# Performance work log

Hardware: AMD Instinct MI355X
Metric: run time of the kernel (lower is better)

## Reference

```python
import jax, jax.numpy as jnp
import numpy as np

M, NC, NT, DX = 8, 1024, 512, 3
CHUNK = 512          # chunk_size
N_STEPS = 8          # n_steps (tol=0.0 -> torch early-stop never fires)
LR = 0.1
B1, B2, EPS = 0.9, 0.999, 1e-8
SQRT5 = 5.0 ** 0.5
LOG2PI = float(np.log(2.0 * np.pi))
NOISE_LB = 1e-4      # gpytorch GreaterThan(1e-4) noise constraint


def setup_inputs():
    key = jax.random.key(0)
    k1, k2, k3 = jax.random.split(key, 3)
    return {
        "xc": jax.random.normal(k1, (M, NC, DX), jnp.float32),
        "yc": jax.random.normal(k2, (M, NC, 1), jnp.float32),
        "xt": jax.random.normal(k3, (M, NT, DX), jnp.float32),
    }


def _kernel(x1, x2, ls, outscale):
    # ScaleKernel(MaternKernel(nu=2.5)); ls: [m,1,1], outscale: [m]
    xs1, xs2 = x1 / ls, x2 / ls
    d2 = (jnp.sum(xs1 * xs1, -1)[:, :, None]
          + jnp.sum(xs2 * xs2, -1)[:, None, :]
          - 2.0 * jnp.einsum('mnd,mkd->mnk', xs1, xs2))
    d2 = jnp.clip(d2, 1e-12, None)   # clamp like gpytorch dist for grad safety
    d = jnp.sqrt(d2)
    k = (1.0 + SQRT5 * d + (5.0 / 3.0) * d2) * jnp.exp(-SQRT5 * d)
    return outscale[:, None, None] * k


def _constrained(params):
    ls = jax.nn.softplus(params["raw_ls"])                          # [m,1,1]
    outscale = jax.nn.softplus(params["raw_os"])                    # [m]
    noise = jax.nn.softplus(params["raw_noise"][:, 0]) + NOISE_LB   # [m]
    return ls, outscale, noise


def _nll(params, x, y):
    # sum over tasks of -ExactMarginalLogLikelihood (gpytorch divides by n)
    ls, outscale, noise = _constrained(params)
    n = x.shape[1]
    K = _kernel(x, x, ls, outscale) + noise[:, None, None] * jnp.eye(n, dtype=x.dtype)
    L = jnp.linalg.cholesky(K)
    diff = y - params["const"][:, None]
    alpha = jax.scipy.linalg.cho_solve((L, True), diff[..., None])[..., 0]
    quad = jnp.sum(diff * alpha, -1)
    logdet = 2.0 * jnp.sum(jnp.log(jnp.diagonal(L, axis1=-2, axis2=-1)), -1)
    mll = -0.5 * (quad + logdet + n * LOG2PI) / n
    return jnp.sum(-mll)


def _adam_step(carry, x_sub, y_sub):
    p, m_, v_, t = carry
    g = jax.grad(_nll)(p, x_sub, y_sub)
    t = t + 1.0
    tm = jax.tree_util.tree_map
    m_ = tm(lambda a, gg: B1 * a + (1.0 - B1) * gg, m_, g)
    v_ = tm(lambda a, gg: B2 * a + (1.0 - B2) * gg * gg, v_, g)
    bc1 = 1.0 - B1 ** t
    bc2 = 1.0 - B2 ** t
    p = tm(lambda pp, mm, vv: pp - LR * (mm / bc1) / (jnp.sqrt(vv / bc2) + EPS), p, m_, v_)
    return (p, m_, v_, t)


def _gp_forward(xc, yc, xt):
    y = yc[..., 0]                                    # [m, nc]
    zl = lambda s: jnp.zeros(s, jnp.float32)
    # gpytorch raw params initialize to 0
    params = {"raw_ls": zl((M, 1, 1)), "raw_os": zl((M,)),
              "raw_noise": zl((M, 1)), "const": zl((M,))}
    m_ = jax.tree_util.tree_map(jnp.zeros_like, params)
    v_ = jax.tree_util.tree_map(jnp.zeros_like, params)
    carry = (params, m_, v_, jnp.float32(0.0))
    for i in range(0, NC, CHUNK):                     # 'Expanding' strategy
        end = min(i + CHUNK, NC)
        x_sub, y_sub = xc[:, :end], y[:, :end]
        step = lambda c, _: (_adam_step(c, x_sub, y_sub), None)
        carry, _ = jax.lax.scan(step, carry, None, length=N_STEPS)
    params = carry[0]
    # posterior predictive with trained hypers (train data = full context)
    ls, outscale, noise = _constrained(params)
    Kcc = _kernel(xc, xc, ls, outscale) + noise[:, None, None] * jnp.eye(NC, dtype=xc.dtype)
    L = jnp.linalg.cholesky(Kcc)
    diff = y - params["const"][:, None]
    alpha = jax.scipy.linalg.cho_solve((L, True), diff[..., None])[..., 0]
    Ktc = _kernel(xt, xc, ls, outscale)               # [m, nt, nc]
    mean = params["const"][:, None] + jnp.einsum('mtn,mn->mt', Ktc, alpha)
    v = jax.scipy.linalg.solve_triangular(L, jnp.swapaxes(Ktc, 1, 2), lower=True)  # [m,nc,nt]
    var_f = outscale[:, None] - jnp.sum(v * v, axis=1)  # Matern(0)=1 -> prior diag = outputscale
    var = var_f + noise[:, None]                      # likelihood(f) adds observation noise
    return jnp.stack([mean, var])                     # [2, m, nt]


def reference(xc, yc, xt):
    return _gp_forward(xc, yc, xt)
```

## Files before the change

kernel.cpp:

```cpp
#include <hip/hip_runtime.h>
#include <math.h>

constexpr int MM = 8;
constexpr int NC = 1024;
constexpr int NT = 512;

constexpr size_t OFF_A     = (size_t)MM * 1024 * 1024;
constexpr size_t OFF_T     = OFF_A * 2;
constexpr size_t OFF_KTC   = OFF_T + (size_t)MM * 512 * 512;
constexpr size_t OFF_ALPHA = OFF_KTC + (size_t)MM * NT * NC;
constexpr size_t OFF_SCAL  = OFF_ALPHA + (size_t)MM * 1024;
constexpr size_t OFF_ACC   = OFF_SCAL + (size_t)MM * 32;
constexpr size_t OFF_CTR   = OFF_ACC + (size_t)MM * 8;

#define S5 2.2360679775f

__device__ __forceinline__ float sigmf(float x) { return 1.0f / (1.0f + expf(-x)); }
__device__ __forceinline__ float softplusf(float x) { return fmaxf(x, 0.0f) + log1pf(expf(-fabsf(x))); }

__device__ __forceinline__ void lt_decode(int x, int& i, int& j) {
  int ii = 0;
  while ((ii + 1) * (ii + 2) / 2 <= x) ++ii;
  i = ii; j = x - ii * (ii + 1) / 2;
}

struct SMem {
  float Ls[64 * 65];
  float Us[64 * 65];
  float Tt[32 * 33];
  float dvec[64];
  float As[16][68];
  float Bs[16][68];
  float xi[64][3];
  float xj[64][3];
  float ai[64];
  float aj[64];
  float red[4][4];
};

template <int TA, int TB>
__device__ __forceinline__ void gemm64(const float* __restrict__ A, int lda,
                                       const float* __restrict__ B, int ldb,
                                       int kBeg, int kEnd, float acc[4][4], SMem& sm) {
  int tid = threadIdx.x, tx = tid & 15, ty = tid >> 4;
  float ra[4], rb[4];
  auto ldAB = [&](int k0) {
#pragma unroll
    for (int q = 0; q < 4; ++q) {
      int e = tid + (q << 8);
      if (TA) { int kk = e >> 6, r = e & 63; ra[q] = A[(size_t)(k0 + kk) * lda + r]; }
      else    { int r = e >> 4, kk = e & 15; ra[q] = A[(size_t)r * lda + k0 + kk]; }
      if (TB) { int c = e >> 4, kk = e & 15; rb[q] = B[(size_t)c * ldb + k0 + kk]; }
      else    { int kk = e >> 6, c = e & 63; rb[q] = B[(size_t)(k0 + kk) * ldb + c]; }
    }
  };
  ldAB(kBeg);
  for (int k0 = kBeg; k0 < kEnd; k0 += 16) {
    __syncthreads();
#pragma unroll
    for (int q = 0; q < 4; ++q) {
      int e = tid + (q << 8);
      if (TA) sm.As[e >> 6][e & 63] = ra[q]; else sm.As[e & 15][e >> 4] = ra[q];
      if (TB) sm.Bs[e & 15][e >> 4] = rb[q]; else sm.Bs[e >> 6][e & 63] = rb[q];
    }
    __syncthreads();
    if (k0 + 16 < kEnd) ldAB(k0 + 16);
#pragma unroll
    for (int kk = 0; kk < 16; ++kk) {
      float a[4], b[4];
#pragma unroll
      for (int i = 0; i < 4; ++i) a[i] = sm.As[kk][ty * 4 + i];
#pragma unroll
      for (int j = 0; j < 4; ++j) b[j] = sm.Bs[kk][tx * 4 + j];
#pragma unroll
      for (int i = 0; i < 4; ++i)
#pragma unroll
        for (int j = 0; j < 4; ++j) acc[i][j] = fmaf(a[i], b[j], acc[i][j]);
    }
  }
}

__device__ void factor64(SMem& sm, float* Uout, int ldu) {
  int tid = threadIdx.x;
  int tx = tid & 15, ty = tid >> 4;
  for (int j = 0; j < 63; ++j) {
    float rinv = 1.0f / sm.Ls[j * 65 + j];
    for (int i = j + 1 + ty; i < 64; i += 16) {
      float lij = sm.Ls[i * 65 + j] * rinv;
      for (int c = j + 1 + tx; c <= i; c += 16) sm.Ls[i * 65 + c] -= lij * sm.Ls[c * 65 + j];
    }
    __syncthreads();
  }
  if (tid < 64) sm.dvec[tid] = 1.0f / sqrtf(sm.Ls[tid * 65 + tid]);
  __syncthreads();
  for (int e = tid; e < 4096; e += 256) { int r = e >> 6, c = e & 63; if (c <= r) sm.Ls[r * 65 + c] *= sm.dvec[c]; }
  __syncthreads();
  for (int e = tid; e < 64 * 65; e += 256) sm.Us[e] = 0.0f;
  __syncthreads();
  if (tid < 64) {
    int b = tid >> 5, c0 = tid & 31, base = b * 32, gc = base + c0;
    sm.Us[gc * 65 + gc] = 1.0f / sm.Ls[gc * 65 + gc];
    for (int r = c0 + 1; r < 32; ++r) {
      int gr = base + r;
      float acc = 0.0f;
      for (int l = c0; l < r; ++l) acc += sm.Ls[gr * 65 + base + l] * sm.Us[(base + l) * 65 + gc];
      sm.Us[gr * 65 + gc] = -acc / sm.Ls[gr * 65 + gr];
    }
  }
  __syncthreads();
  for (int e = tid; e < 1024; e += 256) {
    int r = e >> 5, c = e & 31;
    float acc = 0.0f;
    for (int l = c; l < 32; ++l) acc += sm.Ls[(32 + r) * 65 + l] * sm.Us[l * 65 + c];
    sm.Tt[r * 33 + c] = acc;
  }
  __syncthreads();
  for (int e = tid; e < 1024; e += 256) {
    int r = e >> 5, c = e & 31;
    float acc = 0.0f;
    for (int l = 0; l <= r; ++l) acc += sm.Us[(32 + r) * 65 + 32 + l] * sm.Tt[l * 33 + c];
    sm.Us[(32 + r) * 65 + c] = -acc;
  }
  __syncthreads();
  for (int e = tid; e < 4096; e += 256) { int r = e >> 6, c = e & 63; Uout[(size_t)r * ldu + c] = sm.Us[r * 65 + c]; }
}


__global__ __launch_bounds__(256) void k_init(float* ws) {
  int t = threadIdx.x;
  float* scal = ws + OFF_SCAL;
  float* acc = ws + OFF_ACC;
  if (t < MM) {
    float* s = scal + t * 32;
    for (int i = 0; i < 12; ++i) s[i] = 0.0f;
    float sp0 = 0.69314718056f;
    s[12] = sp0; s[13] = sp0; s[14] = sp0 + 1e-4f; s[15] = 0.0f;
  }
  if (t < MM * 8) acc[t] = 0.0f;
  if (t < MM) ((unsigned*)(ws + OFF_CTR))[t] = 0u;
}

__global__ __launch_bounds__(256) void k_buildK(const float* __restrict__ xc, float* ws, int n) {
  __shared__ SMem sm;
  int job = blockIdx.x, m = blockIdx.y, tid = threadIdx.x;
  const float* xm = xc + (size_t)m * NC * 3;
  float* Km = ws + (size_t)m * 1048576;
  float* Am = ws + OFF_A + (size_t)m * 1048576;
  const float* sT = ws + OFF_SCAL + m * 32;
  float ls = sT[12], os = sT[13], noi = sT[14];
  float il2 = 1.0f / (ls * ls);
  if (job >= 1 && job <= 4) {
    int zi = (job - 1) * 256 + tid;
    if (zi < n) ws[OFF_ALPHA + (size_t)m * 1024 + zi] = 0.0f;
  }
  if (job == 5) {
    if (tid < 4) ws[OFF_ACC + m * 8 + tid] = 0.0f;
    if (tid == 4) ((unsigned*)(ws + OFF_CTR))[m] = 0u;
  }
  int bi, bj; lt_decode(job, bi, bj);
  if (tid < 64) {
    int r = bi * 64 + tid;
    sm.xi[tid][0] = xm[r * 3 + 0]; sm.xi[tid][1] = xm[r * 3 + 1]; sm.xi[tid][2] = xm[r * 3 + 2];
  } else if (tid < 128) {
    int lr = tid - 64; int r = bj * 64 + lr;
    sm.xj[lr][0] = xm[r * 3 + 0]; sm.xj[lr][1] = xm[r * 3 + 1]; sm.xj[lr][2] = xm[r * 3 + 2];
  }
  __syncthreads();
  if (job == 0) {
    for (int e = tid; e < 4096; e += 256) {
      int r = e >> 6, c = e & 63;
      float d0 = sm.xi[r][0] - sm.xj[c][0], d1 = sm.xi[r][1] - sm.xj[c][1], d2 = sm.xi[r][2] - sm.xj[c][2];
      float r2 = d0 * d0 + d1 * d1 + d2 * d2;
      float z = fmaxf(r2 * il2, 1e-12f);
      float dd = sqrtf(z);
      float kv = os * (1.0f + S5 * dd + (5.0f / 3.0f) * z) * __expf(-S5 * dd);
      if (r == c) kv += noi;
      sm.Ls[r * 65 + c] = kv;
    }
    __syncthreads();
    factor64(sm, Am, n);
  } else {
    for (int e = tid; e < 4096; e += 256) {
      int r = e >> 6, c = e & 63;
      float d0 = sm.xi[r][0] - sm.xj[c][0], d1 = sm.xi[r][1] - sm.xj[c][1], d2 = sm.xi[r][2] - sm.xj[c][2];
      float r2 = d0 * d0 + d1 * d1 + d2 * d2;
      float z = fmaxf(r2 * il2, 1e-12f);
      float dd = sqrtf(z);
      float kv = os * (1.0f + S5 * dd + (5.0f / 3.0f) * z) * __expf(-S5 * dd);
      if (bi == bj && r == c) kv += noi;
      Km[(size_t)(bi * 64 + r) * n + bj * 64 + c] = kv;
    }
  }
}

__global__ __launch_bounds__(256) void k_trail(float* ws, int k, int n) {
  __shared__ SMem sm;
  int job = blockIdx.x, m = blockIdx.y, tid = threadIdx.x;
  int tx = tid & 15, ty = tid >> 4;
  float* Km = ws + (size_t)m * 1048576;
  float* Am = ws + OFF_A + (size_t)m * 1048576;
  const float* Linv = Am + (size_t)(k * 64) * n + k * 64;
  int di, dj; lt_decode(job, di, dj);
  int i = k + 1 + di, j = k + 1 + dj;
  float pp[4][4] = {};
  gemm64<0, 1>(Km + (size_t)(i * 64) * n + k * 64, n, Linv, n, 0, 64, pp, sm);
  __syncthreads();
#pragma unroll
  for (int ii = 0; ii < 4; ++ii)
#pragma unroll
    for (int jj = 0; jj < 4; ++jj) sm.Ls[(ty * 4 + ii) * 65 + tx * 4 + jj] = pp[ii][jj];
  if (di == dj) {
    float* P = Am + (size_t)(i * 64) * n + k * 64;
#pragma unroll
    for (int ii = 0; ii < 4; ++ii)
#pragma unroll
      for (int jj = 0; jj < 4; ++jj) P[(size_t)(ty * 4 + ii) * n + tx * 4 + jj] = pp[ii][jj];
  } else {
#pragma unroll
    for (int ii = 0; ii < 4; ++ii)
#pragma unroll
      for (int jj = 0; jj < 4; ++jj) pp[ii][jj] = 0.0f;
    gemm64<0, 1>(Km + (size_t)(j * 64) * n + k * 64, n, Linv, n, 0, 64, pp, sm);
#pragma unroll
    for (int ii = 0; ii < 4; ++ii)
#pragma unroll
      for (int jj = 0; jj < 4; ++jj) sm.Us[(ty * 4 + ii) * 65 + tx * 4 + jj] = pp[ii][jj];
  }
  __syncthreads();
  float acc[4][4] = {};
  {
    const float* Bsrc = (di == dj) ? sm.Ls : sm.Us;
    for (int l = 0; l < 64; ++l) {
      float a[4], b[4];
#pragma unroll
      for (int ii = 0; ii < 4; ++ii) a[ii] = sm.Ls[(ty * 4 + ii) * 65 + l];
#pragma unroll
      for (int jj = 0; jj < 4; ++jj) b[jj] = Bsrc[(tx * 4 + jj) * 65 + l];
#pragma unroll
      for (int ii = 0; ii < 4; ++ii)
#pragma unroll
        for (int jj = 0; jj < 4; ++jj) acc[ii][jj] = fmaf(a[ii], b[jj], acc[ii][jj]);
    }
  }
  float* C = Km + (size_t)(i * 64) * n + j * 64;
  if (job == 0) {
    __syncthreads();
#pragma unroll
    for (int ii = 0; ii < 4; ++ii)
#pragma unroll
      for (int jj = 0; jj < 4; ++jj)
        sm.Ls[(ty * 4 + ii) * 65 + tx * 4 + jj] =
            C[(size_t)(ty * 4 + ii) * n + tx * 4 + jj] - acc[ii][jj];
    __syncthreads();
    factor64(sm, Am + (size_t)((k + 1) * 64) * n + (k + 1) * 64, n);
  } else {
#pragma unroll
    for (int ii = 0; ii < 4; ++ii)
#pragma unroll
      for (int jj = 0; jj < 4; ++jj)
        C[(size_t)(ty * 4 + ii) * n + tx * 4 + jj] -= acc[ii][jj];
  }
}

__global__ __launch_bounds__(256) void k_trinv64(float* ws, int n) {
  __shared__ SMem sm;
  int p = blockIdx.x, m = blockIdx.y, tid = threadIdx.x;
  int tx = tid & 15, ty = tid >> 4;
  float* Am = ws + OFF_A + (size_t)m * 1048576;
  int rb = (2 * p + 1) * 64, cb = 2 * p * 64;
  for (int e = tid; e < 4096; e += 256) {
    int r = e >> 6, c = e & 63;
    sm.Ls[r * 65 + c] = Am[(size_t)(rb + r) * n + cb + c];
    sm.Us[r * 65 + c] = Am[(size_t)(cb + r) * n + cb + c];
  }
  __syncthreads();
  float tt[4][4] = {};
  for (int l = 0; l < 64; ++l) {
    float a[4], b[4];
#pragma unroll
    for (int ii = 0; ii < 4; ++ii) a[ii] = sm.Ls[(ty * 4 + ii) * 65 + l];
#pragma unroll
    for (int jj = 0; jj < 4; ++jj) b[jj] = sm.Us[l * 65 + tx * 4 + jj];
#pragma unroll
    for (int ii = 0; ii < 4; ++ii)
#pragma unroll
      for (int jj = 0; jj < 4; ++jj) tt[ii][jj] = fmaf(a[ii], b[jj], tt[ii][jj]);
  }
  __syncthreads();
#pragma unroll
  for (int ii = 0; ii < 4; ++ii)
#pragma unroll
    for (int jj = 0; jj < 4; ++jj) sm.Ls[(ty * 4 + ii) * 65 + tx * 4 + jj] = tt[ii][jj];
  for (int e = tid; e < 4096; e += 256) {
    int r = e >> 6, c = e & 63;
    sm.Us[r * 65 + c] = Am[(size_t)(rb + r) * n + rb + c];
  }
  __syncthreads();
  float oo[4][4] = {};
  for (int l = 0; l < 64; ++l) {
    float a[4], b[4];
#pragma unroll
    for (int ii = 0; ii < 4; ++ii) a[ii] = sm.Us[(ty * 4 + ii) * 65 + l];
#pragma unroll
    for (int jj = 0; jj < 4; ++jj) b[jj] = sm.Ls[l * 65 + tx * 4 + jj];
#pragma unroll
    for (int ii = 0; ii < 4; ++ii)
#pragma unroll
      for (int jj = 0; jj < 4; ++jj) oo[ii][jj] = fmaf(a[ii], b[jj], oo[ii][jj]);
  }
#pragma unroll
  for (int ii = 0; ii < 4; ++ii)
#pragma unroll
    for (int jj = 0; jj < 4; ++jj)
      Am[(size_t)(rb + ty * 4 + ii) * n + cb + tx * 4 + jj] = -oo[ii][jj];
}

__global__ __launch_bounds__(256) void k_trinvT(float* ws, int s, int n) {
  __shared__ SMem sm;
  int job = blockIdx.x, m = blockIdx.y;
  int tx = threadIdx.x & 15, ty = threadIdx.x >> 4;
  float* Am = ws + OFF_A + (size_t)m * 1048576;
  float* Tm = ws + OFF_T + (size_t)m * 262144;
  int st = s >> 6;
  int p = job / (st * st), rem = job % (st * st);
  int ti = rem / st, tj = rem % st;
  int base = p * 2 * s;
  float acc[4][4] = {};
  gemm64<0, 0>(Am + (size_t)(base + s + ti * 64) * n + base, n,
               Am + (size_t)base * n + base + tj * 64, n, tj * 64, s, acc, sm);
  float* C = Tm + (size_t)p * s * s + (size_t)(ti * 64) * s + tj * 64;
#pragma unroll
  for (int ii = 0; ii < 4; ++ii)
#pragma unroll
    for (int jj = 0; jj < 4; ++jj) C[(size_t)(ty * 4 + ii) * s + tx * 4 + jj] = acc[ii][jj];
}

__global__ __launch_bounds__(256) void k_trinvA(float* ws, int s, int n) {
  __shared__ SMem sm;
  int job = blockIdx.x, m = blockIdx.y;
  int tx = threadIdx.x & 15, ty = threadIdx.x >> 4;
  float* Am = ws + OFF_A + (size_t)m * 1048576;
  const float* Tm = ws + OFF_T + (size_t)m * 262144;
  int st = s >> 6;
  int p = job / (st * st), rem = job % (st * st);
  int ti = rem / st, tj = rem % st;
  int base = p * 2 * s;
  float acc[4][4] = {};
  gemm64<0, 0>(Am + (size_t)(base + s + ti * 64) * n + base + s, n,
               Tm + (size_t)p * s * s + tj * 64, s, 0, (ti + 1) * 64, acc, sm);
  float* C = Am + (size_t)(base + s + ti * 64) * n + base + tj * 64;
#pragma unroll
  for (int ii = 0; ii < 4; ++ii)
#pragma unroll
    for (int jj = 0; jj < 4; ++jj) C[(size_t)(ty * 4 + ii) * n + tx * 4 + jj] = -acc[ii][jj];
}

__global__ __launch_bounds__(256) void k_syrkAT(const float* __restrict__ yc, float* ws, int n) {
  __shared__ SMem sm;
  int job = blockIdx.x, m = blockIdx.y, tid = threadIdx.x;
  int tx = tid & 15, ty = tid >> 4;
  const float* Am = ws + OFF_A + (size_t)m * 1048576;
  float* Gm = ws + (size_t)m * 1048576;
  const float* ym = yc + (size_t)m * NC;
  float* accp = ws + OFF_ACC + m * 8;
  float* al = ws + OFF_ALPHA + (size_t)m * 1024;
  float cm = ws[OFF_SCAL + m * 32 + 15];
  int ib, jb; lt_decode(job, ib, jb);
  if (tid < 64) sm.ai[tid] = ym[ib * 64 + tid] - cm;
  else if (tid < 128) sm.aj[tid - 64] = ym[jb * 64 + tid - 64] - cm;
  float acc[4][4] = {};
  gemm64<1, 0>(Am + ib * 64, n, Am + jb * 64, n, ib * 64, n, acc, sm);
#pragma unroll
  for (int ii = 0; ii < 4; ++ii)
#pragma unroll
    for (int jj = 0; jj < 4; ++jj) {
      int r = ty * 4 + ii, c = tx * 4 + jj;
      Gm[(size_t)(ib * 64 + r) * n + jb * 64 + c] = acc[ii][jj];
      if (ib != jb) Gm[(size_t)(jb * 64 + c) * n + ib * 64 + r] = acc[ii][jj];
    }
  if (ib == jb && tx == ty) {
    atomicAdd(&accp[2], acc[0][0] + acc[1][1] + acc[2][2] + acc[3][3]);
  }
  float rowp[4];
#pragma unroll
  for (int i = 0; i < 4; ++i) {
    float s = 0.0f;
#pragma unroll
    for (int j = 0; j < 4; ++j) s = fmaf(acc[i][j], sm.aj[tx * 4 + j], s);
    rowp[i] = s;
  }
  float colp[4];
  if (ib != jb) {
#pragma unroll
    for (int j = 0; j < 4; ++j) {
      float s = 0.0f;
#pragma unroll
      for (int i = 0; i < 4; ++i) s = fmaf(acc[i][j], sm.ai[ty * 4 + i], s);
      colp[j] = s;
    }
  }
  __syncthreads();
  float* redA = &sm.As[0][0];
  float* redB = &sm.Bs[0][0];
#pragma unroll
  for (int i = 0; i < 4; ++i) redA[(ty * 4 + i) * 16 + tx] = rowp[i];
  if (ib != jb) {
#pragma unroll
    for (int j = 0; j < 4; ++j) redB[(tx * 4 + j) * 16 + ty] = colp[j];
  }
  __syncthreads();
  if (tid < 64) {
    float s = 0.0f;
#pragma unroll
    for (int q = 0; q < 16; ++q) s += redA[tid * 16 + q];
    atomicAdd(&al[ib * 64 + tid], s);
    if (ib != jb) {
      float s2 = 0.0f;
#pragma unroll
      for (int q = 0; q < 16; ++q) s2 += redB[tid * 16 + q];
      atomicAdd(&al[jb * 64 + tid], s2);
    }
  }
}

__global__ __launch_bounds__(256) void k_reduceAD(const float* __restrict__ xc,
                                                  const float* __restrict__ yc,
                                                  float* ws, int n, int tstep) {
  __shared__ SMem sm;
  __shared__ unsigned tkt;
  int job = blockIdx.x, m = blockIdx.y, tid = threadIdx.x;
  const float* xm = xc + (size_t)m * NC * 3;
  const float* Gm = ws + (size_t)m * 1048576;
  const float* al = ws + OFF_ALPHA + (size_t)m * 1024;
  float* accp = ws + OFF_ACC + m * 8;
  float* sT = ws + OFF_SCAL + m * 32;
  int nb = n >> 6;
  int njobs = nb * (nb + 1) / 2;
  float ls = sT[12], os = sT[13];
  float il2 = 1.0f / (ls * ls);
  float c53 = (5.0f / 3.0f) * os / ls;
  int bi, bj; lt_decode(job, bi, bj);
  float w = (bi == bj) ? 1.0f : 2.0f;
  if (tid < 64) {
    int r = bi * 64 + tid;
    sm.xi[tid][0] = xm[r * 3 + 0]; sm.xi[tid][1] = xm[r * 3 + 1]; sm.xi[tid][2] = xm[r * 3 + 2];
    sm.ai[tid] = al[r];
  } else if (tid < 128) {
    int lr = tid - 64; int r = bj * 64 + lr;
    sm.xj[lr][0] = xm[r * 3 + 0]; sm.xj[lr][1] = xm[r * 3 + 1]; sm.xj[lr][2] = xm[r * 3 + 2];
    sm.aj[lr] = al[r];
  }
  __syncthreads();
  float a1 = 0.0f, a2 = 0.0f;
// ... 44 lines not shown
    t6 = sm.red[0][2] + sm.red[1][2] + sm.red[2][2] + sm.red[3][2];
    float T1 = __hip_atomic_fetch_add(&accp[0], 0.0f, __ATOMIC_RELAXED, __HIP_MEMORY_SCOPE_AGENT);
    float T2 = __hip_atomic_fetch_add(&accp[1], 0.0f, __ATOMIC_RELAXED, __HIP_MEMORY_SCOPE_AGENT);
    float t3 = __hip_atomic_fetch_add(&accp[2], 0.0f, __ATOMIC_RELAXED, __HIP_MEMORY_SCOPE_AGENT);
    float noi = sT[14];
    float fn = (float)n;
    float g_ls = 0.5f / fn * (T1 - T2);
    float g_os = 0.5f / (fn * os) * (fn - noi * t3 - t6 + noi * t4);
    float g_no = 0.5f / fn * (t3 - t4);
    float g_c = -t5 / fn;
    float gr[4];
    gr[0] = g_ls * sigmf(sT[0]);
    gr[1] = g_os * sigmf(sT[1]);
    gr[2] = g_no * sigmf(sT[2]);
    gr[3] = g_c;
    float bc1 = 1.0f - powf(0.9f, (float)tstep);
    float bc2 = 1.0f - powf(0.999f, (float)tstep);
#pragma unroll
    for (int i = 0; i < 4; ++i) {
      float mv = 0.9f * sT[4 + i] + 0.1f * gr[i];
      float vv = 0.999f * sT[8 + i] + 0.001f * gr[i] * gr[i];
      sT[4 + i] = mv; sT[8 + i] = vv;
      sT[i] = sT[i] - 0.1f * (mv / bc1) / (sqrtf(vv / bc2) + 1e-8f);
    }
    sT[12] = softplusf(sT[0]);
    sT[13] = softplusf(sT[1]);
    sT[14] = softplusf(sT[2]) + 1e-4f;
    sT[15] = sT[3];
  }
}

__global__ __launch_bounds__(256) void k_buildKtc(const float* __restrict__ xt,
                                                  const float* __restrict__ xc, float* ws) {
  __shared__ SMem sm;
  int job = blockIdx.x, m = blockIdx.y, tid = threadIdx.x;
  const float* xtm = xt + (size_t)m * NT * 3;
  const float* xm = xc + (size_t)m * NC * 3;
  float* Kt = ws + OFF_KTC + (size_t)m * NT * NC;
  float* Tm = ws + OFF_T + (size_t)m * 262144;
  const float* sT = ws + OFF_SCAL + m * 32;
  float ls = sT[12], os = sT[13];
  float il2 = 1.0f / (ls * ls);
  if (job < 2) {
    int z = job * 256 + tid;
    Tm[z] = 0.0f; Tm[NT + z] = 0.0f;
  }
  int ti = job >> 4, tj = job & 15;
  if (tid < 64) {
    int r = ti * 64 + tid;
    sm.xi[tid][0] = xtm[r * 3 + 0]; sm.xi[tid][1] = xtm[r * 3 + 1]; sm.xi[tid][2] = xtm[r * 3 + 2];
  } else if (tid < 128) {
    int lr = tid - 64; int r = tj * 64 + lr;
    sm.xj[lr][0] = xm[r * 3 + 0]; sm.xj[lr][1] = xm[r * 3 + 1]; sm.xj[lr][2] = xm[r * 3 + 2];
  }
  __syncthreads();
  for (int e = tid; e < 4096; e += 256) {
    int r = e >> 6, c = e & 63;
    float d0 = sm.xi[r][0] - sm.xj[c][0], d1 = sm.xi[r][1] - sm.xj[c][1], d2 = sm.xi[r][2] - sm.xj[c][2];
    float r2 = d0 * d0 + d1 * d1 + d2 * d2;
    float z = fmaxf(r2 * il2, 1e-12f);
    float dd = sqrtf(z);
    float kv = os * (1.0f + S5 * dd + (5.0f / 3.0f) * z) * __expf(-S5 * dd);
    Kt[(size_t)(ti * 64 + r) * NC + tj * 64 + c] = kv;
  }
}

__global__ __launch_bounds__(256) void k_predW(float* ws) {
  __shared__ SMem sm;
  int job = blockIdx.x, m = blockIdx.y, tid = threadIdx.x;
  int tx = tid & 15, ty = tid >> 4;
  const float* Kt = ws + OFF_KTC + (size_t)m * NT * NC;
  const float* Gm = ws + (size_t)m * 1048576;
  const float* al = ws + OFF_ALPHA + (size_t)m * 1024;
  float* S1 = ws + OFF_T + (size_t)m * 262144;
  float* S2 = S1 + NT;
  int ti = job >> 4, tj = job & 15;
  if (tid < 64) sm.aj[tid] = al[tj * 64 + tid];
  float acc[4][4] = {};
  gemm64<0, 0>(Kt + (size_t)(ti * 64) * NC, NC, Gm + tj * 64, 1024, 0, 1024, acc, sm);
  float s1p[4], s2p[4];
#pragma unroll
  for (int i = 0; i < 4; ++i) {
    float a1 = 0.0f, a2 = 0.0f;
    const float* kr = Kt + (size_t)(ti * 64 + ty * 4 + i) * NC + tj * 64;
#pragma unroll
    for (int j = 0; j < 4; ++j) {
      float kv = kr[tx * 4 + j];
      a1 = fmaf(kv, sm.aj[tx * 4 + j], a1);
      a2 = fmaf(kv, acc[i][j], a2);
    }
    s1p[i] = a1; s2p[i] = a2;
// ... 10 lines not shown
  if (tid < 64) {
    float a1 = 0.0f, a2 = 0.0f;
#pragma unroll
    for (int q = 0; q < 16; ++q) { a1 += redA[tid * 16 + q]; a2 += redB[tid * 16 + q]; }
    atomicAdd(&S1[ti * 64 + tid], a1);
    atomicAdd(&S2[ti * 64 + tid], a2);
  }
}

__global__ __launch_bounds__(256) void k_final(float* ws, float* out) {
  int m = blockIdx.y, t = blockIdx.x * 256 + threadIdx.x;
  const float* S1 = ws + OFF_T + (size_t)m * 262144;
  const float* S2 = S1 + NT;
  const float* sT = ws + OFF_SCAL + m * 32;
  if (t < NT) {
    out[(size_t)m * NT + t] = sT[15] + S1[t];
    out[(size_t)MM * NT + (size_t)m * NT + t] = sT[13] + sT[14] - S2[t];
  }
}

extern "C" void kernel_launch(void* const* d_in, const int* in_sizes, int n_in,
                              void* d_out, int out_size, void* d_ws, size_t ws_size,
                              hipStream_t stream) {
  const float* xc = (const float*)d_in[0];
  const float* yc = (const float*)d_in[1];
  const float* xt = (const float*)d_in[2];
  float* out = (float*)d_out;
  float* ws = (float*)d_ws;

  k_init<<<dim3(1), dim3(256), 0, stream>>>(ws);

  for (int step = 0; step < 17; ++step) {
    int n = step < 8 ? 512 : 1024;
    int nb = n >> 6;
    k_buildK<<<dim3(nb * (nb + 1) / 2, MM), dim3(256), 0, stream>>>(xc, ws, n);
    for (int k = 0; k <= nb - 2; ++k) {
      int t = nb - 1 - k;
      k_trail<<<dim3(t * (t + 1) / 2, MM), dim3(256), 0, stream>>>(ws, k, n);
    }
    k_trinv64<<<dim3(n / 128, MM), dim3(256), 0, stream>>>(ws, n);
    for (int s = 128; s < n; s <<= 1) {
      int st = s >> 6, np = n / (2 * s);
      k_trinvT<<<dim3(np * st * st, MM), dim3(256), 0, stream>>>(ws, s, n);
      k_trinvA<<<dim3(np * st * st, MM), dim3(256), 0, stream>>>(ws, s, n);
    }
    k_syrkAT<<<dim3(nb * (nb + 1) / 2, MM), dim3(256), 0, stream>>>(yc, ws, n);
    if (step < 16) {
      k_reduceAD<<<dim3(nb * (nb + 1) / 2, MM), dim3(256), 0, stream>>>(xc, yc, ws, n, step + 1);
    }
  }

  k_buildKtc<<<dim3(128, MM), dim3(256), 0, stream>>>(xt, xc, ws);
  k_predW<<<dim3(128, MM), dim3(256), 0, stream>>>(ws);
  k_final<<<dim3(2, MM), dim3(256), 0, stream>>>(ws, out);

  (void)in_sizes; (void)n_in; (void)out_size; (void)ws_size;
}
```

Measured before the change: 20.51 ms.

## Switch Cholesky, triangular inverse and SYRK to 128-wide blocks

```diff
diff --git a/kernel.cpp b/kernel.cpp
--- a/kernel.cpp
+++ b/kernel.cpp
@@ -38,6 +38,22 @@
   float red[4][4];
 };
 
+struct SMem128 {
+  float As[16][132];
+  float Bs[16][132];
+  float ai[128];
+  float aj[128];
+  float red[4][4];
+};
+
+struct FactBuf {
+  float Ls[64 * 65];
+  float Us[64 * 65];
+  float P[64 * 65];
+  float Tt[32 * 33];
+  float dvec[64];
+};
+
 template <int TA, int TB>
 __device__ __forceinline__ void gemm64(const float* __restrict__ A, int lda,
                                        const float* __restrict__ B, int ldb,
@@ -80,49 +96,185 @@
   }
 }
 
-__device__ void factor64(SMem& sm, float* Uout, int ldu) {
+template <int TA, int TB>
+__device__ __forceinline__ void gemm128(const float* __restrict__ A, int lda,
+                                        const float* __restrict__ B, int ldb,
+                                        int kBeg, int kEnd, float acc[8][8], SMem128& sm) {
+  int tid = threadIdx.x, tx = tid & 15, ty = tid >> 4;
+  float ra[8], rb[8];
+  auto ldAB = [&](int k0) {
+#pragma unroll
+    for (int q = 0; q < 8; ++q) {
+      int e = tid + (q << 8);
+      if (TA) { int kk = e >> 7, r = e & 127; ra[q] = A[(size_t)(k0 + kk) * lda + r]; }
+      else    { int r = e >> 4, kk = e & 15;  ra[q] = A[(size_t)r * lda + k0 + kk]; }
+      if (TB) { int c = e >> 4, kk = e & 15;  rb[q] = B[(size_t)c * ldb + k0 + kk]; }
+      else    { int kk = e >> 7, c = e & 127; rb[q] = B[(size_t)(k0 + kk) * ldb + c]; }
+    }
+  };
+  ldAB(kBeg);
+  for (int k0 = kBeg; k0 < kEnd; k0 += 16) {
+    __syncthreads();
+#pragma unroll
+    for (int q = 0; q < 8; ++q) {
+      int e = tid + (q << 8);
+      if (TA) sm.As[e >> 7][e & 127] = ra[q]; else sm.As[e & 15][e >> 4] = ra[q];
+      if (TB) sm.Bs[e & 15][e >> 4] = rb[q];  else sm.Bs[e >> 7][e & 127] = rb[q];
+    }
+    __syncthreads();
+    if (k0 + 16 < kEnd) ldAB(k0 + 16);
+#pragma unroll
+    for (int kk = 0; kk < 16; ++kk) {
+      float a[8], b[8];
+#pragma unroll
+      for (int i = 0; i < 8; ++i) a[i] = sm.As[kk][ty * 8 + i];
+#pragma unroll
+      for (int j = 0; j < 8; ++j) b[j] = sm.Bs[kk][tx * 8 + j];
+#pragma unroll
+      for (int i = 0; i < 8; ++i)
+#pragma unroll
+        for (int j = 0; j < 8; ++j) acc[i][j] = fmaf(a[i], b[j], acc[i][j]);
+    }
+  }
+}
+
+__device__ void f64_inlds(float* Ls, float* Us, float* Tt, float* dvec,
+                          float* Uout, int ldu) {
   int tid = threadIdx.x;
   int tx = tid & 15, ty = tid >> 4;
   for (int j = 0; j < 63; ++j) {
-    float rinv = 1.0f / sm.Ls[j * 65 + j];
+    float rinv = 1.0f / Ls[j * 65 + j];
     for (int i = j + 1 + ty; i < 64; i += 16) {
-      float lij = sm.Ls[i * 65 + j] * rinv;
-      for (int c = j + 1 + tx; c <= i; c += 16) sm.Ls[i * 65 + c] -= lij * sm.Ls[c * 65 + j];
+      float lij = Ls[i * 65 + j] * rinv;
+      for (int c = j + 1 + tx; c <= i; c += 16) Ls[i * 65 + c] -= lij * Ls[c * 65 + j];
     }
     __syncthreads();
   }
-  if (tid < 64) sm.dvec[tid] = 1.0f / sqrtf(sm.Ls[tid * 65 + tid]);
-  __syncthreads();
-  for (int e = tid; e < 4096; e += 256) { int r = e >> 6, c = e & 63; if (c <= r) sm.Ls[r * 65 + c] *= sm.dvec[c]; }
-  __syncthreads();
-  for (int e = tid; e < 64 * 65; e += 256) sm.Us[e] = 0.0f;
+  if (tid < 64) dvec[tid] = 1.0f / sqrtf(Ls[tid * 65 + tid]);
+  __syncthreads();
+  for (int e = tid; e < 4096; e += 256) { int r = e >> 6, c = e & 63; if (c <= r) Ls[r * 65 + c] *= dvec[c]; }
+  __syncthreads();
+  for (int e = tid; e < 64 * 65; e += 256) Us[e] = 0.0f;
   __syncthreads();
   if (tid < 64) {
     int b = tid >> 5, c0 = tid & 31, base = b * 32, gc = base + c0;
-    sm.Us[gc * 65 + gc] = 1.0f / sm.Ls[gc * 65 + gc];
+    Us[gc * 65 + gc] = 1.0f / Ls[gc * 65 + gc];
     for (int r = c0 + 1; r < 32; ++r) {
       int gr = base + r;
       float acc = 0.0f;
-      for (int l = c0; l < r; ++l) acc += sm.Ls[gr * 65 + base + l] * sm.Us[(base + l) * 65 + gc];
-      sm.Us[gr * 65 + gc] = -acc / sm.Ls[gr * 65 + gr];
+      for (int l = c0; l < r; ++l) acc += Ls[gr * 65 + base + l] * Us[(base + l) * 65 + gc];
+      Us[gr * 65 + gc] = -acc / Ls[gr * 65 + gr];
     }
   }
   __syncthreads();
   for (int e = tid; e < 1024; e += 256) {
     int r = e >> 5, c = e & 31;
     float acc = 0.0f;
-    for (int l = c; l < 32; ++l) acc += sm.Ls[(32 + r) * 65 + l] * sm.Us[l * 65 + c];
-    sm.Tt[r * 33 + c] = acc;
+    for (int l = c; l < 32; ++l) acc += Ls[(32 + r) * 65 + l] * Us[l * 65 + c];
+    Tt[r * 33 + c] = acc;
   }
   __syncthreads();
   for (int e = tid; e < 1024; e += 256) {
     int r = e >> 5, c = e & 31;
     float acc = 0.0f;
-    for (int l = 0; l <= r; ++l) acc += sm.Us[(32 + r) * 65 + 32 + l] * sm.Tt[l * 33 + c];
-    sm.Us[(32 + r) * 65 + c] = -acc;
-  }
-  __syncthreads();
-  for (int e = tid; e < 4096; e += 256) { int r = e >> 6, c = e & 63; Uout[(size_t)r * ldu + c] = sm.Us[r * 65 + c]; }
+    for (int l = 0; l <= r; ++l) acc += Us[(32 + r) * 65 + 32 + l] * Tt[l * 33 + c];
+    Us[(32 + r) * 65 + c] = -acc;
+  }
+  __syncthreads();
+  for (int e = tid; e < 4096; e += 256) { int r = e >> 6, c = e & 63; Uout[(size_t)r * ldu + c] = Us[r * 65 + c]; }
+}
+
+__device__ void factor128dev(FactBuf& fb, float* Km, float* Am, int r0, int n) {
+  int tid = threadIdx.x, tx = tid & 15, ty = tid >> 4;
+  for (int e = tid; e < 4096; e += 256) { int r = e >> 6, c = e & 63; fb.Ls[r * 65 + c] = Km[(size_t)(r0 + r) * n + r0 + c]; }
+  __syncthreads();
+  f64_inlds(fb.Ls, fb.Us, fb.Tt, fb.dvec, Am + (size_t)r0 * n + r0, n);
+  for (int e = tid; e < 4096; e += 256) { int r = e >> 6, c = e & 63; fb.P[r * 65 + c] = Km[(size_t)(r0 + 64 + r) * n + r0 + c]; }
+  __syncthreads();
+  {
+    float res[4][4] = {};
+    for (int l = 0; l < 64; ++l) {
+      float a[4], b[4];
+#pragma unroll
+      for (int ii = 0; ii < 4; ++ii) a[ii] = fb.P[(ty * 4 + ii) * 65 + l];
+#pragma unroll
+      for (int jj = 0; jj < 4; ++jj) b[jj] = fb.Us[(tx * 4 + jj) * 65 + l];
+#pragma unroll
+      for (int ii = 0; ii < 4; ++ii)
+#pragma unroll
+        for (int jj = 0; jj < 4; ++jj) res[ii][jj] = fmaf(a[ii], b[jj], res[ii][jj]);
+    }
+    __syncthreads();
+#pragma unroll
+    for (int ii = 0; ii < 4; ++ii)
+#pragma unroll
+      for (int jj = 0; jj < 4; ++jj) fb.P[(ty * 4 + ii) * 65 + tx * 4 + jj] = res[ii][jj];
+  }
+  __syncthreads();
+  for (int e = tid; e < 4096; e += 256) { int r = e >> 6, c = e & 63; fb.Ls[r * 65 + c] = Km[(size_t)(r0 + 64 + r) * n + r0 + 64 + c]; }
+  __syncthreads();
+  {
+    float acc[4][4] = {};
+    for (int l = 0; l < 64; ++l) {
+      float a[4], b[4];
+#pragma unroll
+      for (int ii = 0; ii < 4; ++ii) a[ii] = fb.P[(ty * 4 + ii) * 65 + l];
+#pragma unroll
+      for (int jj = 0; jj < 4; ++jj) b[jj] = fb.P[(tx * 4 + jj) * 65 + l];
+#pragma unroll
+      for (int ii = 0; ii < 4; ++ii)
+#pragma unroll
+        for (int jj = 0; jj < 4; ++jj) acc[ii][jj] = fmaf(a[ii], b[jj], acc[ii][jj]);
+    }
+#pragma unroll
+    for (int ii = 0; ii < 4; ++ii)
+#pragma unroll
+      for (int jj = 0; jj < 4; ++jj) fb.Ls[(ty * 4 + ii) * 65 + tx * 4 + jj] -= acc[ii][jj];
+  }
+  __syncthreads();
+  f64_inlds(fb.Ls, fb.Us, fb.Tt, fb.dvec, Am + (size_t)(r0 + 64) * n + r0 + 64, n);
+  for (int e = tid; e < 4096; e += 256) { int r = e >> 6, c = e & 63; fb.Ls[r * 65 + c] = Am[(size_t)(r0 + r) * n + r0 + c]; }
+  __syncthreads();
+  {
+    float res[4][4] = {};
+    for (int l = 0; l < 64; ++l) {
+      float a[4], b[4];
+#pragma unroll
+      for (int ii = 0; ii < 4; ++ii) a[ii] = fb.P[(ty * 4 + ii) * 65 + l];
+#pragma unroll
+      for (int jj = 0; jj < 4; ++jj) b[jj] = fb.Ls[l * 65 + tx * 4 + jj];
+#pragma unroll
+      for (int ii = 0; ii < 4; ++ii)
+#pragma unroll
+        for (int jj = 0; jj < 4; ++jj) res[ii][jj] = fmaf(a[ii], b[jj], res[ii][jj]);
+    }
+    __syncthreads();
+#pragma unroll
+    for (int ii = 0; ii < 4; ++ii)
+#pragma unroll
+      for (int jj = 0; jj < 4; ++jj) fb.P[(ty * 4 + ii) * 65 + tx * 4 + jj] = res[ii][jj];
+  }
+  __syncthreads();
+  {
+    float res[4][4] = {};
+    for (int l = 0; l < 64; ++l) {
+      float a[4], b[4];
+#pragma unroll
+      for (int ii = 0; ii < 4; ++ii) a[ii] = fb.Us[(ty * 4 + ii) * 65 + l];
+#pragma unroll
+      for (int jj = 0; jj < 4; ++jj) b[jj] = fb.P[l * 65 + tx * 4 + jj];
+#pragma unroll
+      for (int ii = 0; ii < 4; ++ii)
+#pragma unroll
+        for (int jj = 0; jj < 4; ++jj) res[ii][jj] = fmaf(a[ii], b[jj], res[ii][jj]);
+    }
+#pragma unroll
+    for (int ii = 0; ii < 4; ++ii)
+#pragma unroll
+      for (int jj = 0; jj < 4; ++jj)
+        Am[(size_t)(r0 + 64 + ty * 4 + ii) * n + r0 + tx * 4 + jj] = -res[ii][jj];
+  }
+  for (int e = tid; e < 4096; e += 256) { int r = e >> 6, c = e & 63; Am[(size_t)(r0 + r) * n + r0 + 64 + c] = 0.0f; }
 }
 
 
@@ -141,11 +293,10 @@
 }
 
 __global__ __launch_bounds__(256) void k_buildK(const float* __restrict__ xc, float* ws, int n) {
-  __shared__ SMem sm;
+  __shared__ float xi[64][3], xj[64][3];
   int job = blockIdx.x, m = blockIdx.y, tid = threadIdx.x;
   const float* xm = xc + (size_t)m * NC * 3;
   float* Km = ws + (size_t)m * 1048576;
-  float* Am = ws + OFF_A + (size_t)m * 1048576;
   const float* sT = ws + OFF_SCAL + m * 32;
   float ls = sT[12], os = sT[13], noi = sT[14];
   float il2 = 1.0f / (ls * ls);
@@ -160,203 +311,111 @@
   int bi, bj; lt_decode(job, bi, bj);
   if (tid < 64) {
     int r = bi * 64 + tid;
-    sm.xi[tid][0] = xm[r * 3 + 0]; sm.xi[tid][1] = xm[r * 3 + 1]; sm.xi[tid][2] = xm[r * 3 + 2];
+    xi[tid][0] = xm[r * 3 + 0]; xi[tid][1] = xm[r * 3 + 1]; xi[tid][2] = xm[r * 3 + 2];
   } else if (tid < 128) {
     int lr = tid - 64; int r = bj * 64 + lr;
-    sm.xj[lr][0] = xm[r * 3 + 0]; sm.xj[lr][1] = xm[r * 3 + 1]; sm.xj[lr][2] = xm[r * 3 + 2];
-  }
-  __syncthreads();
-  if (job == 0) {
-    for (int e = tid; e < 4096; e += 256) {
-      int r = e >> 6, c = e & 63;
-      float d0 = sm.xi[r][0] - sm.xj[c][0], d1 = sm.xi[r][1] - sm.xj[c][1], d2 = sm.xi[r][2] - sm.xj[c][2];
-      float r2 = d0 * d0 + d1 * d1 + d2 * d2;
-      float z = fmaxf(r2 * il2, 1e-12f);
-      float dd = sqrtf(z);
-      float kv = os * (1.0f + S5 * dd + (5.0f / 3.0f) * z) * __expf(-S5 * dd);
-      if (r == c) kv += noi;
-      sm.Ls[r * 65 + c] = kv;
-    }
-    __syncthreads();
-    factor64(sm, Am, n);
-  } else {
-    for (int e = tid; e < 4096; e += 256) {
-      int r = e >> 6, c = e & 63;
-      float d0 = sm.xi[r][0] - sm.xj[c][0], d1 = sm.xi[r][1] - sm.xj[c][1], d2 = sm.xi[r][2] - sm.xj[c][2];
-      float r2 = d0 * d0 + d1 * d1 + d2 * d2;
-      float z = fmaxf(r2 * il2, 1e-12f);
-      float dd = sqrtf(z);
-      float kv = os * (1.0f + S5 * dd + (5.0f / 3.0f) * z) * __expf(-S5 * dd);
-      if (bi == bj && r == c) kv += noi;
-      Km[(size_t)(bi * 64 + r) * n + bj * 64 + c] = kv;
-    }
-  }
-}
-
-__global__ __launch_bounds__(256) void k_trail(float* ws, int k, int n) {
-  __shared__ SMem sm;
-  int job = blockIdx.x, m = blockIdx.y, tid = threadIdx.x;
-  int tx = tid & 15, ty = tid >> 4;
+    xj[lr][0] = xm[r * 3 + 0]; xj[lr][1] = xm[r * 3 + 1]; xj[lr][2] = xm[r * 3 + 2];
+  }
+  __syncthreads();
+  for (int e = tid; e < 4096; e += 256) {
+    int r = e >> 6, c = e & 63;
+    float d0 = xi[r][0] - xj[c][0], d1 = xi[r][1] - xj[c][1], d2 = xi[r][2] - xj[c][2];
+    float r2 = d0 * d0 + d1 * d1 + d2 * d2;
+    float z = fmaxf(r2 * il2, 1e-12f);
+    float dd = sqrtf(z);
+    float kv = os * (1.0f + S5 * dd + (5.0f / 3.0f) * z) * __expf(-S5 * dd);
+    if (bi == bj && r == c) kv += noi;
+    Km[(size_t)(bi * 64 + r) * n + bj * 64 + c] = kv;
+  }
+}
+
+__global__ __launch_bounds__(256) void k_factor128(float* ws, int kk, int n) {
+  __shared__ FactBuf fb;
+  int m = blockIdx.x;
+  factor128dev(fb, ws + (size_t)m * 1048576, ws + OFF_A + (size_t)m * 1048576, kk * 128, n);
+}
+
+__global__ __launch_bounds__(256) void k_panel128(float* ws, int k, int n) {
+  __shared__ SMem128 sm;
+  int m = blockIdx.y, i = k + 1 + blockIdx.x;
+  int tx = threadIdx.x & 15, ty = threadIdx.x >> 4;
   float* Km = ws + (size_t)m * 1048576;
   float* Am = ws + OFF_A + (size_t)m * 1048576;
-  const float* Linv = Am + (size_t)(k * 64) * n + k * 64;
+  float acc[8][8] = {};
+  gemm128<0, 1>(Km + (size_t)(i * 128) * n + k * 128, n,
+                Am + (size_t)(k * 128) * n + k * 128, n, 0, 128, acc, sm);
+  float* P = Am + (size_t)(i * 128) * n + k * 128;
+#pragma unroll
+  for (int ii = 0; ii < 8; ++ii)
+#pragma unroll
+    for (int jj = 0; jj < 8; ++jj) P[(size_t)(ty * 8 + ii) * n + tx * 8 + jj] = acc[ii][jj];
+}
+
+__global__ __launch_bounds__(256) void k_trailF128(float* ws, int k, int n) {
+  __shared__ union { SMem128 g; FactBuf f; } sm;
+  int job = blockIdx.x, m = blockIdx.y;
+  int tx = threadIdx.x & 15, ty = threadIdx.x >> 4;
+  float* Km = ws + (size_t)m * 1048576;
+  float* Am = ws + OFF_A + (size_t)m * 1048576;
   int di, dj; lt_decode(job, di, dj);
   int i = k + 1 + di, j = k + 1 + dj;
-  float pp[4][4] = {};
-  gemm64<0, 1>(Km + (size_t)(i * 64) * n + k * 64, n, Linv, n, 0, 64, pp, sm);
-  __syncthreads();
-#pragma unroll
-  for (int ii = 0; ii < 4; ++ii)
-#pragma unroll
-    for (int jj = 0; jj < 4; ++jj) sm.Ls[(ty * 4 + ii) * 65 + tx * 4 + jj] = pp[ii][jj];
-  if (di == dj) {
-    float* P = Am + (size_t)(i * 64) * n + k * 64;
-#pragma unroll
-    for (int ii = 0; ii < 4; ++ii)
-#pragma unroll
-      for (int jj = 0; jj < 4; ++jj) P[(size_t)(ty * 4 + ii) * n + tx * 4 + jj] = pp[ii][jj];
-  } else {
-#pragma unroll
-    for (int ii = 0; ii < 4; ++ii)
-#pragma unroll
-      for (int jj = 0; jj < 4; ++jj) pp[ii][jj] = 0.0f;
-    gemm64<0, 1>(Km + (size_t)(j * 64) * n + k * 64, n, Linv, n, 0, 64, pp, sm);
-#pragma unroll
-    for (int ii = 0; ii < 4; ++ii)
-#pragma unroll
-      for (int jj = 0; jj < 4; ++jj) sm.Us[(ty * 4 + ii) * 65 + tx * 4 + jj] = pp[ii][jj];
-  }
-  __syncthreads();
-  float acc[4][4] = {};
-  {
-    const float* Bsrc = (di == dj) ? sm.Ls : sm.Us;
-    for (int l = 0; l < 64; ++l) {
-      float a[4], b[4];
-#pragma unroll
-      for (int ii = 0; ii < 4; ++ii) a[ii] = sm.Ls[(ty * 4 + ii) * 65 + l];
-#pragma unroll
-      for (int jj = 0; jj < 4; ++jj) b[jj] = Bsrc[(tx * 4 + jj) * 65 + l];
-#pragma unroll
-      for (int ii = 0; ii < 4; ++ii)
-#pragma unroll
-        for (int jj = 0; jj < 4; ++jj) acc[ii][jj] = fmaf(a[ii], b[jj], acc[ii][jj]);
-    }
-  }
-  float* C = Km + (size_t)(i * 64) * n + j * 64;
+  float acc[8][8] = {};
+  gemm128<0, 1>(Am + (size_t)(i * 128) * n + k * 128, n,
+                Am + (size_t)(j * 128) * n + k * 128, n, 0, 128, acc, sm.g);
+  float* C = Km + (size_t)(i * 128) * n + j * 128;
+#pragma unroll
+  for (int ii = 0; ii < 8; ++ii)
+#pragma unroll
+    for (int jj = 0; jj < 8; ++jj)
+      C[(size_t)(ty * 8 + ii) * n + tx * 8 + jj] -= acc[ii][jj];
   if (job == 0) {
     __syncthreads();
-#pragma unroll
-    for (int ii = 0; ii < 4; ++ii)
-#pragma unroll
-      for (int jj = 0; jj < 4; ++jj)
-        sm.Ls[(ty * 4 + ii) * 65 + tx * 4 + jj] =
-            C[(size_t)(ty * 4 + ii) * n + tx * 4 + jj] - acc[ii][jj];
-    __syncthreads();
-    factor64(sm, Am + (size_t)((k + 1) * 64) * n + (k + 1) * 64, n);
-  } else {
-#pragma unroll
-    for (int ii = 0; ii < 4; ++ii)
-#pragma unroll
-      for (int jj = 0; jj < 4; ++jj)
-        C[(size_t)(ty * 4 + ii) * n + tx * 4 + jj] -= acc[ii][jj];
-  }
-}
-
-__global__ __launch_bounds__(256) void k_trinv64(float* ws, int n) {
-  __shared__ SMem sm;
-  int p = blockIdx.x, m = blockIdx.y, tid = threadIdx.x;
-  int tx = tid & 15, ty = tid >> 4;
-  float* Am = ws + OFF_A + (size_t)m * 1048576;
-  int rb = (2 * p + 1) * 64, cb = 2 * p * 64;
-  for (int e = tid; e < 4096; e += 256) {
-    int r = e >> 6, c = e & 63;
-    sm.Ls[r * 65 + c] = Am[(size_t)(rb + r) * n + cb + c];
-    sm.Us[r * 65 + c] = Am[(size_t)(cb + r) * n + cb + c];
-  }
-  __syncthreads();
-  float tt[4][4] = {};
-  for (int l = 0; l < 64; ++l) {
-    float a[4], b[4];
-#pragma unroll
-    for (int ii = 0; ii < 4; ++ii) a[ii] = sm.Ls[(ty * 4 + ii) * 65 + l];
-#pragma unroll
-    for (int jj = 0; jj < 4; ++jj) b[jj] = sm.Us[l * 65 + tx * 4 + jj];
-#pragma unroll
-    for (int ii = 0; ii < 4; ++ii)
-#pragma unroll
-      for (int jj = 0; jj < 4; ++jj) tt[ii][jj] = fmaf(a[ii], b[jj], tt[ii][jj]);
-  }
-  __syncthreads();
-#pragma unroll
-  for (int ii = 0; ii < 4; ++ii)
-#pragma unroll
-    for (int jj = 0; jj < 4; ++jj) sm.Ls[(ty * 4 + ii) * 65 + tx * 4 + jj] = tt[ii][jj];
-  for (int e = tid; e < 4096; e += 256) {
-    int r = e >> 6, c = e & 63;
-    sm.Us[r * 65 + c] = Am[(size_t)(rb + r) * n + rb + c];
-  }
-  __syncthreads();
-  float oo[4][4] = {};
-  for (int l = 0; l < 64; ++l) {
-    float a[4], b[4];
-#pragma unroll
-    for (int ii = 0; ii < 4; ++ii) a[ii] = sm.Us[(ty * 4 + ii) * 65 + l];
-#pragma unroll
-    for (int jj = 0; jj < 4; ++jj) b[jj] = sm.Ls[l * 65 + tx * 4 + jj];
-#pragma unroll
-    for (int ii = 0; ii < 4; ++ii)
-#pragma unroll
-      for (int jj = 0; jj < 4; ++jj) oo[ii][jj] = fmaf(a[ii], b[jj], oo[ii][jj]);
-  }
-#pragma unroll
-  for (int ii = 0; ii < 4; ++ii)
-#pragma unroll
-    for (int jj = 0; jj < 4; ++jj)
-      Am[(size_t)(rb + ty * 4 + ii) * n + cb + tx * 4 + jj] = -oo[ii][jj];
+    factor128dev(sm.f, Km, Am, (k + 1) * 128, n);
+  }
 }
 
 __global__ __launch_bounds__(256) void k_trinvT(float* ws, int s, int n) {
-  __shared__ SMem sm;
+  __shared__ SMem128 sm;
   int job = blockIdx.x, m = blockIdx.y;
   int tx = threadIdx.x & 15, ty = threadIdx.x >> 4;
   float* Am = ws + OFF_A + (size_t)m * 1048576;
   float* Tm = ws + OFF_T + (size_t)m * 262144;
-  int st = s >> 6;
+  int st = s >> 7;
   int p = job / (st * st), rem = job % (st * st);
   int ti = rem / st, tj = rem % st;
   int base = p * 2 * s;
-  float acc[4][4] = {};
-  gemm64<0, 0>(Am + (size_t)(base + s + ti * 64) * n + base, n,
-               Am + (size_t)base * n + base + tj * 64, n, tj * 64, s, acc, sm);
-  float* C = Tm + (size_t)p * s * s + (size_t)(ti * 64) * s + tj * 64;
-#pragma unroll
-  for (int ii = 0; ii < 4; ++ii)
-#pragma unroll
-    for (int jj = 0; jj < 4; ++jj) C[(size_t)(ty * 4 + ii) * s + tx * 4 + jj] = acc[ii][jj];
+  float acc[8][8] = {};
+  gemm128<0, 0>(Am + (size_t)(base + s + ti * 128) * n + base, n,
+                Am + (size_t)base * n + base + tj * 128, n, tj * 128, s, acc, sm);
+  float* C = Tm + (size_t)p * s * s + (size_t)(ti * 128) * s + tj * 128;
+#pragma unroll
+  for (int ii = 0; ii < 8; ++ii)
+#pragma unroll
+    for (int jj = 0; jj < 8; ++jj) C[(size_t)(ty * 8 + ii) * s + tx * 8 + jj] = acc[ii][jj];
 }
 
 __global__ __launch_bounds__(256) void k_trinvA(float* ws, int s, int n) {
-  __shared__ SMem sm;
+  __shared__ SMem128 sm;
   int job = blockIdx.x, m = blockIdx.y;
   int tx = threadIdx.x & 15, ty = threadIdx.x >> 4;
   float* Am = ws + OFF_A + (size_t)m * 1048576;
   const float* Tm = ws + OFF_T + (size_t)m * 262144;
-  int st = s >> 6;
+  int st = s >> 7;
   int p = job / (st * st), rem = job % (st * st);
   int ti = rem / st, tj = rem % st;
   int base = p * 2 * s;
-  float acc[4][4] = {};
-  gemm64<0, 0>(Am + (size_t)(base + s + ti * 64) * n + base + s, n,
-               Tm + (size_t)p * s * s + tj * 64, s, 0, (ti + 1) * 64, acc, sm);
-  float* C = Am + (size_t)(base + s + ti * 64) * n + base + tj * 64;
-#pragma unroll
-  for (int ii = 0; ii < 4; ++ii)
-#pragma unroll
-    for (int jj = 0; jj < 4; ++jj) C[(size_t)(ty * 4 + ii) * n + tx * 4 + jj] = -acc[ii][jj];
+  float acc[8][8] = {};
+  gemm128<0, 0>(Am + (size_t)(base + s + ti * 128) * n + base + s, n,
+                Tm + (size_t)p * s * s + tj * 128, s, 0, (ti + 1) * 128, acc, sm);
+  float* C = Am + (size_t)(base + s + ti * 128) * n + base + tj * 128;
+#pragma unroll
+  for (int ii = 0; ii < 8; ++ii)
+#pragma unroll
+    for (int jj = 0; jj < 8; ++jj) C[(size_t)(ty * 8 + ii) * n + tx * 8 + jj] = -acc[ii][jj];
 }
 
 __global__ __launch_bounds__(256) void k_syrkAT(const float* __restrict__ yc, float* ws, int n) {
-  __shared__ SMem sm;
+  __shared__ SMem128 sm;
   int job = blockIdx.x, m = blockIdx.y, tid = threadIdx.x;
   int tx = tid & 15, ty = tid >> 4;
   const float* Am = ws + OFF_A + (size_t)m * 1048576;
@@ -366,36 +425,39 @@
   float* al = ws + OFF_ALPHA + (size_t)m * 1024;
   float cm = ws[OFF_SCAL + m * 32 + 15];
   int ib, jb; lt_decode(job, ib, jb);
-  if (tid < 64) sm.ai[tid] = ym[ib * 64 + tid] - cm;
-  else if (tid < 128) sm.aj[tid - 64] = ym[jb * 64 + tid - 64] - cm;
-  float acc[4][4] = {};
-  gemm64<1, 0>(Am + ib * 64, n, Am + jb * 64, n, ib * 64, n, acc, sm);
-#pragma unroll
-  for (int ii = 0; ii < 4; ++ii)
-#pragma unroll
-    for (int jj = 0; jj < 4; ++jj) {
-      int r = ty * 4 + ii, c = tx * 4 + jj;
-      Gm[(size_t)(ib * 64 + r) * n + jb * 64 + c] = acc[ii][jj];
-      if (ib != jb) Gm[(size_t)(jb * 64 + c) * n + ib * 64 + r] = acc[ii][jj];
+  if (tid < 128) sm.ai[tid] = ym[ib * 128 + tid] - cm;
+  else sm.aj[tid - 128] = ym[jb * 128 + tid - 128] - cm;
+  float acc[8][8] = {};
+  gemm128<1, 0>(Am + ib * 128, n, Am + jb * 128, n, ib * 128, n, acc, sm);
+#pragma unroll
+  for (int ii = 0; ii < 8; ++ii)
+#pragma unroll
+    for (int jj = 0; jj < 8; ++jj) {
+      int r = ty * 8 + ii, c = tx * 8 + jj;
+      Gm[(size_t)(ib * 128 + r) * n + jb * 128 + c] = acc[ii][jj];
+      if (ib != jb) Gm[(size_t)(jb * 128 + c) * n + ib * 128 + r] = acc[ii][jj];
     }
   if (ib == jb && tx == ty) {
-    atomicAdd(&accp[2], acc[0][0] + acc[1][1] + acc[2][2] + acc[3][3]);
-  }
-  float rowp[4];
-#pragma unroll
-  for (int i = 0; i < 4; ++i) {
+    float td = 0.0f;
+#pragma unroll
+    for (int ii = 0; ii < 8; ++ii) td += acc[ii][ii];
+    atomicAdd(&accp[2], td);
+  }
+  float rowp[8];
+#pragma unroll
+  for (int i = 0; i < 8; ++i) {
     float s = 0.0f;
 #pragma unroll
-    for (int j = 0; j < 4; ++j) s = fmaf(acc[i][j], sm.aj[tx * 4 + j], s);
+    for (int j = 0; j < 8; ++j) s = fmaf(acc[i][j], sm.aj[tx * 8 + j], s);
     rowp[i] = s;
   }
-  float colp[4];
+  float colp[8];
   if (ib != jb) {
 #pragma unroll
-    for (int j = 0; j < 4; ++j) {
+    for (int j = 0; j < 8; ++j) {
       float s = 0.0f;
 #pragma unroll
-      for (int i = 0; i < 4; ++i) s = fmaf(acc[i][j], sm.ai[ty * 4 + i], s);
+      for (int i = 0; i < 8; ++i) s = fmaf(acc[i][j], sm.ai[ty * 8 + i], s);
       colp[j] = s;
     }
   }
@@ -403,22 +465,22 @@
   float* redA = &sm.As[0][0];
   float* redB = &sm.Bs[0][0];
 #pragma unroll
-  for (int i = 0; i < 4; ++i) redA[(ty * 4 + i) * 16 + tx] = rowp[i];
+  for (int i = 0; i < 8; ++i) redA[(ty * 8 + i) * 16 + tx] = rowp[i];
   if (ib != jb) {
 #pragma unroll
-    for (int j = 0; j < 4; ++j) redB[(tx * 4 + j) * 16 + ty] = colp[j];
-  }
-  __syncthreads();
-  if (tid < 64) {
+    for (int j = 0; j < 8; ++j) redB[(tx * 8 + j) * 16 + ty] = colp[j];
+  }
+  __syncthreads();
+  if (tid < 128) {
     float s = 0.0f;
 #pragma unroll
     for (int q = 0; q < 16; ++q) s += redA[tid * 16 + q];
-    atomicAdd(&al[ib * 64 + tid], s);
+    atomicAdd(&al[ib * 128 + tid], s);
     if (ib != jb) {
       float s2 = 0.0f;
 #pragma unroll
       for (int q = 0; q < 16; ++q) s2 += redB[tid * 16 + q];
-      atomicAdd(&al[jb * 64 + tid], s2);
+      atomicAdd(&al[jb * 128 + tid], s2);
     }
   }
 }
@@ -529,7 +591,7 @@
 
 __global__ __launch_bounds__(256) void k_buildKtc(const float* __restrict__ xt,
                                                   const float* __restrict__ xc, float* ws) {
-  __shared__ SMem sm;
+  __shared__ float xi[64][3], xj[64][3];
   int job = blockIdx.x, m = blockIdx.y, tid = threadIdx.x;
   const float* xtm = xt + (size_t)m * NT * 3;
   const float* xm = xc + (size_t)m * NC * 3;
@@ -545,15 +607,15 @@
   int ti = job >> 4, tj = job & 15;
   if (tid < 64) {
     int r = ti * 64 + tid;
-    sm.xi[tid][0] = xtm[r * 3 + 0]; sm.xi[tid][1] = xtm[r * 3 + 1]; sm.xi[tid][2] = xtm[r * 3 + 2];
+    xi[tid][0] = xtm[r * 3 + 0]; xi[tid][1] = xtm[r * 3 + 1]; xi[tid][2] = xtm[r * 3 + 2];
   } else if (tid < 128) {
     int lr = tid - 64; int r = tj * 64 + lr;
-    sm.xj[lr][0] = xm[r * 3 + 0]; sm.xj[lr][1] = xm[r * 3 + 1]; sm.xj[lr][2] = xm[r * 3 + 2];
+    xj[lr][0] = xm[r * 3 + 0]; xj[lr][1] = xm[r * 3 + 1]; xj[lr][2] = xm[r * 3 + 2];
   }
   __syncthreads();
   for (int e = tid; e < 4096; e += 256) {
     int r = e >> 6, c = e & 63;
-    float d0 = sm.xi[r][0] - sm.xj[c][0], d1 = sm.xi[r][1] - sm.xj[c][1], d2 = sm.xi[r][2] - sm.xj[c][2];
+    float d0 = xi[r][0] - xj[c][0], d1 = xi[r][1] - xj[c][1], d2 = xi[r][2] - xj[c][2];
     float r2 = d0 * d0 + d1 * d1 + d2 * d2;
     float z = fmaxf(r2 * il2, 1e-12f);
     float dd = sqrtf(z);
@@ -630,19 +692,20 @@
 
   for (int step = 0; step < 17; ++step) {
     int n = step < 8 ? 512 : 1024;
-    int nb = n >> 6;
+    int nb = n >> 6, nb128 = n >> 7;
     k_buildK<<<dim3(nb * (nb + 1) / 2, MM), dim3(256), 0, stream>>>(xc, ws, n);
-    for (int k = 0; k <= nb - 2; ++k) {
-      int t = nb - 1 - k;
-      k_trail<<<dim3(t * (t + 1) / 2, MM), dim3(256), 0, stream>>>(ws, k, n);
-    }
-    k_trinv64<<<dim3(n / 128, MM), dim3(256), 0, stream>>>(ws, n);
+    k_factor128<<<dim3(MM), dim3(256), 0, stream>>>(ws, 0, n);
+    for (int k = 0; k <= nb128 - 2; ++k) {
+      int t = nb128 - 1 - k;
+      k_panel128<<<dim3(t, MM), dim3(256), 0, stream>>>(ws, k, n);
+      k_trailF128<<<dim3(t * (t + 1) / 2, MM), dim3(256), 0, stream>>>(ws, k, n);
+    }
     for (int s = 128; s < n; s <<= 1) {
-      int st = s >> 6, np = n / (2 * s);
+      int st = s >> 7, np = n / (2 * s);
       k_trinvT<<<dim3(np * st * st, MM), dim3(256), 0, stream>>>(ws, s, n);
       k_trinvA<<<dim3(np * st * st, MM), dim3(256), 0, stream>>>(ws, s, n);
     }
-    k_syrkAT<<<dim3(nb * (nb + 1) / 2, MM), dim3(256), 0, stream>>>(yc, ws, n);
+    k_syrkAT<<<dim3(nb128 * (nb128 + 1) / 2, MM), dim3(256), 0, stream>>>(yc, ws, n);
     if (step < 16) {
       k_reduceAD<<<dim3(nb * (nb + 1) / 2, MM), dim3(256), 0, stream>>>(xc, yc, ws, n, step + 1);
     }
```

Result: slower. 32.11 ms (+56.6%).
